# Kernel tuning notes

Measured on AMD Instinct MI355X. Metric: run time of the kernel, lower is better.

Reference implementation:

```python
import jax, jax.numpy as jnp
import numpy as np

N = 16384
D_IN = 64
D_HID = D_IN // 2  # 32
D_OUT = 32


def setup_inputs() -> dict:
    key = jax.random.key(0)
    kA, kX, k1, k2, k3 = jax.random.split(key, 5)
    # Dense adjacency-like operator [N, N]; scaled so activations stay sane.
    A = jax.random.normal(kA, (N, N), dtype=jnp.float32) / np.sqrt(N)
    X = jax.random.normal(kX, (N, D_IN), dtype=jnp.float32)
    # torch nn.Linear weights: [out_features, in_features], no bias
    W1 = jax.random.normal(k1, (D_IN, D_IN), dtype=jnp.float32) / np.sqrt(D_IN)
    W2 = jax.random.normal(k2, (D_HID, D_IN), dtype=jnp.float32) / np.sqrt(D_IN)
    W3 = jax.random.normal(k3, (D_OUT, D_HID), dtype=jnp.float32) / np.sqrt(D_HID)
    return {"A": A, "X": X, "W1": W1, "W2": W2, "W3": W3}


def reference(A, X, W1, W2, W3):
    # Layer 1: relu(fc1(A @ X)); fc(x) = x @ W.T
    h = jax.nn.relu((A @ X) @ W1.T)        # [N, D_IN]
    # Layer 2: relu(fc2(A @ h))
    h = jax.nn.relu((A @ h) @ W2.T)        # [N, D_HID]
    # Layer 3: fc3(A @ h), no activation
    return (A @ h) @ W3.T                  # [N, D_OUT]
```

## Files before the change

kernel.cpp:

```cpp
#include <hip/hip_runtime.h>
#include <cstdint>
#include <cstddef>


#define NN 16384
#define SPLITK 8
#define KCHUNK (NN / SPLITK)

typedef __attribute__((ext_vector_type(8))) short s16x8;
typedef __attribute__((ext_vector_type(4))) float fx4;

__device__ __forceinline__ unsigned short f2bf_rne(float f) {
    unsigned int x = __builtin_bit_cast(unsigned int, f);
    x += 0x7fffu + ((x >> 16) & 1u);
    return (unsigned short)(x >> 16);
}

__device__ __forceinline__ s16x8 pack_bf(fx4 a, fx4 b) {
    s16x8 t;
    t[0] = (short)f2bf_rne(a[0]);
    t[1] = (short)f2bf_rne(a[1]);
    t[2] = (short)f2bf_rne(a[2]);
    t[3] = (short)f2bf_rne(a[3]);
    t[4] = (short)f2bf_rne(b[0]);
    t[5] = (short)f2bf_rne(b[1]);
    t[6] = (short)f2bf_rne(b[2]);
    t[7] = (short)f2bf_rne(b[3]);
    return t;
}

template <int D, int AMODE>
__global__ __launch_bounds__(256, 4) void k_spmm(
    const float* __restrict__ A32,
    const unsigned short* __restrict__ Abf_r,
    unsigned short* __restrict__ Abf_w,
    const unsigned short* __restrict__ PT,
    float* __restrict__ part)
{
    const int lane = threadIdx.x & 63;
    const int wv   = threadIdx.x >> 6;
    const int srow = lane & 15;
    const int kg   = lane >> 4;
    const int s    = blockIdx.y;
    const long kbeg = (long)s * KCHUNK;
    const int rowbase = blockIdx.x * 128 + wv * 32;
    const long r0 = rowbase + srow;
    const long r1 = rowbase + 16 + srow;

    fx4 acc0[D / 16], acc1[D / 16];
#pragma unroll
    for (int c = 0; c < D / 16; ++c) {
        acc0[c] = (fx4){0.f, 0.f, 0.f, 0.f};
        acc1[c] = (fx4){0.f, 0.f, 0.f, 0.f};
    }

#pragma unroll 2
    for (int i = 0; i < KCHUNK / 32; ++i) {
        const long ko = kbeg + (long)i * 32;
        s16x8 af0, af1;
        if (AMODE == 2) {
            af0 = __builtin_nontemporal_load((const s16x8*)(Abf_r + r0 * (long)NN + ko + kg * 8));
            af1 = __builtin_nontemporal_load((const s16x8*)(Abf_r + r1 * (long)NN + ko + kg * 8));
        } else {
            const float* p0 = A32 + r0 * (long)NN + ko + kg * 4;
            const float* p1 = A32 + r1 * (long)NN + ko + kg * 4;
            fx4 a00 = __builtin_nontemporal_load((const fx4*)p0);
            fx4 a01 = __builtin_nontemporal_load((const fx4*)(p0 + 16));
            fx4 a10 = __builtin_nontemporal_load((const fx4*)p1);
            fx4 a11 = __builtin_nontemporal_load((const fx4*)(p1 + 16));
            af0 = pack_bf(a00, a01);
            af1 = pack_bf(a10, a11);
            if (AMODE == 1) {
                __builtin_nontemporal_store(af0, (s16x8*)(Abf_w + r0 * (long)NN + ko + kg * 8));
                __builtin_nontemporal_store(af1, (s16x8*)(Abf_w + r1 * (long)NN + ko + kg * 8));
            }
        }
#pragma unroll
        for (int c = 0; c < D / 16; ++c) {
            s16x8 bf = *(const s16x8*)(PT + (long)(c * 16 + srow) * NN + ko + kg * 8);
            acc0[c] = __builtin_amdgcn_mfma_f32_16x16x32_bf16(af0, bf, acc0[c], 0, 0, 0);
            acc1[c] = __builtin_amdgcn_mfma_f32_16x16x32_bf16(af1, bf, acc1[c], 0, 0, 0);
        }
    }

    float* pbase = part + (long)s * NN * D;
#pragma unroll
    for (int c = 0; c < D / 16; ++c) {
#pragma unroll
        for (int r = 0; r < 4; ++r) {
            pbase[(long)(rowbase + kg * 4 + r) * D + c * 16 + srow]      = acc0[c][r];
            pbase[(long)(rowbase + 16 + kg * 4 + r) * D + c * 16 + srow] = acc1[c][r];
        }
    }
}

template <int DIN, int DOUT, int NSUM, bool RELU>
__global__ __launch_bounds__(256) void k_proj(
    const float* __restrict__ src,
    const float* __restrict__ W,
    unsigned short* __restrict__ PT)
{
    __shared__ float Ws[DOUT * DIN];
    __shared__ float Hs[64][DIN + 1];
    const int tid = threadIdx.x;
    for (int i = tid; i < DOUT * DIN; i += 256) Ws[i] = W[i];
    const int rbase = blockIdx.x * 64;
    for (int i = tid; i < 64 * DIN; i += 256) {
        const int rl = i / DIN, k = i % DIN;
        float v = 0.f;
#pragma unroll
        for (int s2 = 0; s2 < NSUM; ++s2)
            v += src[(long)s2 * NN * DIN + (long)(rbase + rl) * DIN + k];
        Hs[rl][k] = RELU ? fmaxf(v, 0.f) : v;
    }
    __syncthreads();
    const int rl = tid & 63;
    const int c0 = tid >> 6;
    const int r  = rbase + rl;
    const int kk = r & 31;
    const int pidx = (r & ~31) + ((kk & 15) >> 2) * 8 + (kk & 3) + ((kk >> 4) << 2);
    for (int c = c0; c < DOUT; c += 4) {
        float accv = 0.f;
#pragma unroll
        for (int k = 0; k < DIN; ++k) accv += Hs[rl][k] * Ws[c * DIN + k];
        PT[(long)c * NN + pidx] = f2bf_rne(accv);
    }
}

__global__ __launch_bounds__(256) void k_red(
    const float* __restrict__ part, float* __restrict__ out)
{
    const int e = blockIdx.x * 256 + threadIdx.x;
    if (e >= NN * 32 / 4) return;
    fx4 v = (fx4){0.f, 0.f, 0.f, 0.f};
#pragma unroll
    for (int s = 0; s < SPLITK; ++s)
        v += __builtin_nontemporal_load((const fx4*)(part + (long)s * NN * 32 + (long)e * 4));
    *(fx4*)(out + (long)e * 4) = v;
}

extern "C" void kernel_launch(void* const* d_in, const int* in_sizes, int n_in,
                              void* d_out, int out_size, void* d_ws, size_t ws_size,
                              hipStream_t stream) {
    const float* A  = (const float*)d_in[0];
    const float* X  = (const float*)d_in[1];
    const float* W1 = (const float*)d_in[2];
    const float* W2 = (const float*)d_in[3];
    const float* W3 = (const float*)d_in[4];
    float* out = (float*)d_out;

    char* ws = (char*)d_ws;
    const size_t part_b = (size_t)SPLITK * NN * 64 * 4;
    const size_t pt_b   = (size_t)64 * NN * 2;
    const size_t abf_b  = (size_t)NN * NN * 2;
    float*          part = (float*)ws;
    unsigned short* PT   = (unsigned short*)(ws + part_b);
    unsigned short* Abf  = (unsigned short*)(ws + part_b + pt_b);
    const bool save = ws_size >= part_b + pt_b + abf_b;

    dim3 b(256);
    dim3 gP(NN / 64);
    dim3 gG(NN / 128, SPLITK);

    k_proj<64, 64, 1, false><<<gP, b, 0, stream>>>(X, W1, PT);
    if (save) k_spmm<64, 1><<<gG, b, 0, stream>>>(A, nullptr, Abf, PT, part);
    else      k_spmm<64, 0><<<gG, b, 0, stream>>>(A, nullptr, nullptr, PT, part);

    k_proj<64, 32, SPLITK, true><<<gP, b, 0, stream>>>(part, W2, PT);
    if (save) k_spmm<32, 2><<<gG, b, 0, stream>>>(nullptr, Abf, nullptr, PT, part);
    else      k_spmm<32, 0><<<gG, b, 0, stream>>>(A, nullptr, nullptr, PT, part);

    k_proj<32, 32, SPLITK, true><<<gP, b, 0, stream>>>(part, W3, PT);
    if (save) k_spmm<32, 2><<<gG, b, 0, stream>>>(nullptr, Abf, nullptr, PT, part);
    else      k_spmm<32, 0><<<gG, b, 0, stream>>>(A, nullptr, nullptr, PT, part);

    k_red<<<dim3(NN * 32 / 4 / 256), b, 0, stream>>>(part, out);
}
```

Measured before the change: 821.5 us.

## Fuse all GCN stages into one persistent cooperative kernel with grid syncs

Replaces the seven separate launches (three projections, three split-K SpMMs, one reduction) with a single persistent cooperative kernel. Phases are separated by grid-wide barriers and work units are distributed with grid-stride loops. Layers 2 and 3 now use split-K of 16 with 64-row wave tiles, so each PT fragment is reused across four A tiles. This removes launch gaps and tail effects, at the cost of grid-sync overhead, a persistent grid capped by occupancy, and a larger partial-sum reduction.

```diff
diff --git a/kernel.cpp b/kernel.cpp
--- a/kernel.cpp
+++ b/kernel.cpp
@@ -1,11 +1,16 @@
 #include <hip/hip_runtime.h>
+#include <hip/hip_cooperative_groups.h>
 #include <cstdint>
 #include <cstddef>
 
+namespace cg = cooperative_groups;
+
 
 #define NN 16384
-#define SPLITK 8
-#define KCHUNK (NN / SPLITK)
+#define SK1 8
+#define KC1 (NN / SK1)
+#define SK2 16
+#define KC2 (NN / SK2)
 
 typedef __attribute__((ext_vector_type(8))) short s16x8;
 typedef __attribute__((ext_vector_type(4))) float fx4;
@@ -29,114 +34,185 @@
     return t;
 }
 
-template <int D, int AMODE>
-__global__ __launch_bounds__(256, 4) void k_spmm(
-    const float* __restrict__ A32,
-    const unsigned short* __restrict__ Abf_r,
-    unsigned short* __restrict__ Abf_w,
-    const unsigned short* __restrict__ PT,
-    float* __restrict__ part)
-{
-    const int lane = threadIdx.x & 63;
-    const int wv   = threadIdx.x >> 6;
-    const int srow = lane & 15;
-    const int kg   = lane >> 4;
-    const int s    = blockIdx.y;
-    const long kbeg = (long)s * KCHUNK;
-    const int rowbase = blockIdx.x * 128 + wv * 32;
-    const long r0 = rowbase + srow;
-    const long r1 = rowbase + 16 + srow;
-
-    fx4 acc0[D / 16], acc1[D / 16];
-#pragma unroll
-    for (int c = 0; c < D / 16; ++c) {
-        acc0[c] = (fx4){0.f, 0.f, 0.f, 0.f};
-        acc1[c] = (fx4){0.f, 0.f, 0.f, 0.f};
-    }
-
+template <int DIN, int DOUT, int NSUM, bool RELU>
+__device__ __forceinline__ void proj_phase(
+    const float* __restrict__ src, const float* __restrict__ W,
+    unsigned short* __restrict__ PT, float* Ws, float* Hs,
+    int nblk, int bid, int tid)
+{
+    for (int i = tid; i < DOUT * DIN; i += 256) Ws[i] = W[i];
+    for (int rb = bid; rb < NN / 16; rb += nblk) {
+        const int rbase = rb * 16;
+        __syncthreads();
+        for (int i = tid; i < 16 * DIN; i += 256) {
+            const int rl = i / DIN, k = i % DIN;
+            float v = 0.f;
+#pragma unroll
+            for (int s2 = 0; s2 < NSUM; ++s2)
+                v += src[(long)s2 * NN * DIN + (long)(rbase + rl) * DIN + k];
+            Hs[rl * 65 + k] = RELU ? fmaxf(v, 0.f) : v;
+        }
+        __syncthreads();
+        const int rl = tid & 15;
+        const int r = rbase + rl;
+        const int kk = r & 31;
+        const int pidx = (r & ~31) + ((kk & 15) >> 2) * 8 + (kk & 3) + ((kk >> 4) << 2);
+        for (int c = tid >> 4; c < DOUT; c += 16) {
+            float acc = 0.f;
+#pragma unroll
+            for (int k = 0; k < DIN; ++k) acc += Hs[rl * 65 + k] * Ws[c * DIN + k];
+            PT[(long)c * NN + pidx] = f2bf_rne(acc);
+        }
+    }
+}
+
+template <int SAVE>
+__device__ __forceinline__ void spmm1_phase(
+    const float* __restrict__ A32, unsigned short* __restrict__ Abf,
+    const unsigned short* __restrict__ PT, float* __restrict__ part,
+    int nblk, int bid, int wv, int srow, int kg)
+{
+    for (int wu = bid; wu < (NN / 128) * SK1; wu += nblk) {
+        const int rb = wu & (NN / 128 - 1);
+        const int s  = wu >> 7;
+        const long kbeg = (long)s * KC1;
+        const int rowbase = rb * 128 + wv * 32;
+        const long r0 = rowbase + srow;
+        const long r1 = rowbase + 16 + srow;
+
+        fx4 acc0[4], acc1[4];
+#pragma unroll
+        for (int c = 0; c < 4; ++c) {
+            acc0[c] = (fx4){0.f, 0.f, 0.f, 0.f};
+            acc1[c] = (fx4){0.f, 0.f, 0.f, 0.f};
+        }
 #pragma unroll 2
-    for (int i = 0; i < KCHUNK / 32; ++i) {
-        const long ko = kbeg + (long)i * 32;
-        s16x8 af0, af1;
-        if (AMODE == 2) {
-            af0 = __builtin_nontemporal_load((const s16x8*)(Abf_r + r0 * (long)NN + ko + kg * 8));
-            af1 = __builtin_nontemporal_load((const s16x8*)(Abf_r + r1 * (long)NN + ko + kg * 8));
-        } else {
+        for (int i = 0; i < KC1 / 32; ++i) {
+            const long ko = kbeg + (long)i * 32;
             const float* p0 = A32 + r0 * (long)NN + ko + kg * 4;
             const float* p1 = A32 + r1 * (long)NN + ko + kg * 4;
             fx4 a00 = __builtin_nontemporal_load((const fx4*)p0);
             fx4 a01 = __builtin_nontemporal_load((const fx4*)(p0 + 16));
             fx4 a10 = __builtin_nontemporal_load((const fx4*)p1);
             fx4 a11 = __builtin_nontemporal_load((const fx4*)(p1 + 16));
-            af0 = pack_bf(a00, a01);
-            af1 = pack_bf(a10, a11);
-            if (AMODE == 1) {
-                __builtin_nontemporal_store(af0, (s16x8*)(Abf_w + r0 * (long)NN + ko + kg * 8));
-                __builtin_nontemporal_store(af1, (s16x8*)(Abf_w + r1 * (long)NN + ko + kg * 8));
-            }
-        }
-#pragma unroll
-        for (int c = 0; c < D / 16; ++c) {
-            s16x8 bf = *(const s16x8*)(PT + (long)(c * 16 + srow) * NN + ko + kg * 8);
-            acc0[c] = __builtin_amdgcn_mfma_f32_16x16x32_bf16(af0, bf, acc0[c], 0, 0, 0);
-            acc1[c] = __builtin_amdgcn_mfma_f32_16x16x32_bf16(af1, bf, acc1[c], 0, 0, 0);
-        }
-    }
-
-    float* pbase = part + (long)s * NN * D;
-#pragma unroll
-    for (int c = 0; c < D / 16; ++c) {
-#pragma unroll
-        for (int r = 0; r < 4; ++r) {
-            pbase[(long)(rowbase + kg * 4 + r) * D + c * 16 + srow]      = acc0[c][r];
-            pbase[(long)(rowbase + 16 + kg * 4 + r) * D + c * 16 + srow] = acc1[c][r];
-        }
-    }
-}
-
-template <int DIN, int DOUT, int NSUM, bool RELU>
-__global__ __launch_bounds__(256) void k_proj(
-    const float* __restrict__ src,
-    const float* __restrict__ W,
-    unsigned short* __restrict__ PT)
-{
-    __shared__ float Ws[DOUT * DIN];
-    __shared__ float Hs[64][DIN + 1];
-    const int tid = threadIdx.x;
-    for (int i = tid; i < DOUT * DIN; i += 256) Ws[i] = W[i];
-    const int rbase = blockIdx.x * 64;
-    for (int i = tid; i < 64 * DIN; i += 256) {
-        const int rl = i / DIN, k = i % DIN;
-        float v = 0.f;
-#pragma unroll
-        for (int s2 = 0; s2 < NSUM; ++s2)
-            v += src[(long)s2 * NN * DIN + (long)(rbase + rl) * DIN + k];
-        Hs[rl][k] = RELU ? fmaxf(v, 0.f) : v;
-    }
-    __syncthreads();
-    const int rl = tid & 63;
-    const int c0 = tid >> 6;
-    const int r  = rbase + rl;
-    const int kk = r & 31;
-    const int pidx = (r & ~31) + ((kk & 15) >> 2) * 8 + (kk & 3) + ((kk >> 4) << 2);
-    for (int c = c0; c < DOUT; c += 4) {
-        float accv = 0.f;
-#pragma unroll
-        for (int k = 0; k < DIN; ++k) accv += Hs[rl][k] * Ws[c * DIN + k];
-        PT[(long)c * NN + pidx] = f2bf_rne(accv);
-    }
-}
-
-__global__ __launch_bounds__(256) void k_red(
-    const float* __restrict__ part, float* __restrict__ out)
-{
-    const int e = blockIdx.x * 256 + threadIdx.x;
-    if (e >= NN * 32 / 4) return;
-    fx4 v = (fx4){0.f, 0.f, 0.f, 0.f};
-#pragma unroll
-    for (int s = 0; s < SPLITK; ++s)
-        v += __builtin_nontemporal_load((const fx4*)(part + (long)s * NN * 32 + (long)e * 4));
-    *(fx4*)(out + (long)e * 4) = v;
+            s16x8 af0 = pack_bf(a00, a01);
+            s16x8 af1 = pack_bf(a10, a11);
+            if (SAVE) {
+                __builtin_nontemporal_store(af0, (s16x8*)(Abf + r0 * (long)NN + ko + kg * 8));
+                __builtin_nontemporal_store(af1, (s16x8*)(Abf + r1 * (long)NN + ko + kg * 8));
+            }
+#pragma unroll
+            for (int c = 0; c < 4; ++c) {
+                s16x8 bf = *(const s16x8*)(PT + (long)(c * 16 + srow) * NN + ko + kg * 8);
+                acc0[c] = __builtin_amdgcn_mfma_f32_16x16x32_bf16(af0, bf, acc0[c], 0, 0, 0);
+                acc1[c] = __builtin_amdgcn_mfma_f32_16x16x32_bf16(af1, bf, acc1[c], 0, 0, 0);
+            }
+        }
+        float* pbase = part + (long)s * NN * 64;
+#pragma unroll
+        for (int c = 0; c < 4; ++c)
+#pragma unroll
+            for (int r = 0; r < 4; ++r) {
+                pbase[(long)(rowbase + kg * 4 + r) * 64 + c * 16 + srow]      = acc0[c][r];
+                pbase[(long)(rowbase + 16 + kg * 4 + r) * 64 + c * 16 + srow] = acc1[c][r];
+            }
+    }
+}
+
+template <int ABF>
+__device__ __forceinline__ void spmm2_phase(
+    const unsigned short* __restrict__ Abf, const float* __restrict__ A32,
+    const unsigned short* __restrict__ PT, float* __restrict__ part,
+    int nblk, int bid, int wv, int srow, int kg)
+{
+    for (int wu = bid; wu < (NN / 256) * SK2; wu += nblk) {
+        const int rb = wu & (NN / 256 - 1);
+        const int s  = wu >> 6;
+        const long kbeg = (long)s * KC2;
+        const int rowbase = rb * 256 + wv * 64;
+
+        fx4 acc[4][2];
+#pragma unroll
+        for (int t = 0; t < 4; ++t)
+#pragma unroll
+            for (int c = 0; c < 2; ++c) acc[t][c] = (fx4){0.f, 0.f, 0.f, 0.f};
+
+#pragma unroll 2
+        for (int i = 0; i < KC2 / 32; ++i) {
+            const long ko = kbeg + (long)i * 32;
+            s16x8 af[4];
+            if (ABF) {
+#pragma unroll
+                for (int t = 0; t < 4; ++t)
+                    af[t] = *(const s16x8*)(Abf + (long)(rowbase + t * 16 + srow) * NN + ko + kg * 8);
+            } else {
+#pragma unroll
+                for (int t = 0; t < 4; ++t) {
+                    const float* p = A32 + (long)(rowbase + t * 16 + srow) * NN + ko + kg * 4;
+                    fx4 a0 = __builtin_nontemporal_load((const fx4*)p);
+                    fx4 a1 = __builtin_nontemporal_load((const fx4*)(p + 16));
+                    af[t] = pack_bf(a0, a1);
+                }
+            }
+            s16x8 b0 = *(const s16x8*)(PT + (long)srow * NN + ko + kg * 8);
+            s16x8 b1 = *(const s16x8*)(PT + (long)(16 + srow) * NN + ko + kg * 8);
+#pragma unroll
+            for (int t = 0; t < 4; ++t) {
+                acc[t][0] = __builtin_amdgcn_mfma_f32_16x16x32_bf16(af[t], b0, acc[t][0], 0, 0, 0);
+                acc[t][1] = __builtin_amdgcn_mfma_f32_16x16x32_bf16(af[t], b1, acc[t][1], 0, 0, 0);
+            }
+        }
+        float* pbase = part + (long)s * NN * 32;
+#pragma unroll
+        for (int t = 0; t < 4; ++t)
+#pragma unroll
+            for (int c = 0; c < 2; ++c)
+#pragma unroll
+                for (int r = 0; r < 4; ++r)
+                    pbase[(long)(rowbase + t * 16 + kg * 4 + r) * 32 + c * 16 + srow] = acc[t][c][r];
+    }
+}
+
+__device__ __forceinline__ void red_phase(
+    const float* __restrict__ part, float* __restrict__ out, int nthr, int gtid)
+{
+    for (int e = gtid; e < NN * 32 / 4; e += nthr) {
+        fx4 v = (fx4){0.f, 0.f, 0.f, 0.f};
+#pragma unroll
+        for (int s = 0; s < SK2; ++s)
+            v += *(const fx4*)(part + (long)s * NN * 32 + (long)e * 4);
+        *(fx4*)(out + (long)e * 4) = v;
+    }
+}
+
+template <int SAVE>
+__global__ __launch_bounds__(256, 4) void gcn_fused(
+    const float* __restrict__ A32, const float* __restrict__ X,
+    const float* __restrict__ W1, const float* __restrict__ W2,
+    const float* __restrict__ W3, float* __restrict__ out,
+    float* __restrict__ part, unsigned short* __restrict__ PT,
+    unsigned short* __restrict__ Abf)
+{
+    __shared__ float Ws[64 * 64];
+    __shared__ float Hs[16 * 65];
+    cg::grid_group g = cg::this_grid();
+    const int tid = threadIdx.x, bid = blockIdx.x, nblk = gridDim.x;
+    const int lane = tid & 63, wv = tid >> 6;
+    const int srow = lane & 15, kg = lane >> 4;
+
+    proj_phase<64, 64, 1, false>(X, W1, PT, Ws, Hs, nblk, bid, tid);
+    __threadfence(); g.sync();
+    spmm1_phase<SAVE>(A32, Abf, PT, part, nblk, bid, wv, srow, kg);
+    __threadfence(); g.sync();
+    proj_phase<64, 32, SK1, true>(part, W2, PT, Ws, Hs, nblk, bid, tid);
+    __threadfence(); g.sync();
+    spmm2_phase<SAVE>(Abf, A32, PT, part, nblk, bid, wv, srow, kg);
+    __threadfence(); g.sync();
+    proj_phase<32, 32, SK2, true>(part, W3, PT, Ws, Hs, nblk, bid, tid);
+    __threadfence(); g.sync();
+    spmm2_phase<SAVE>(Abf, A32, PT, part, nblk, bid, wv, srow, kg);
+    __threadfence(); g.sync();
+    red_phase(part, out, nblk * 256, bid * 256 + tid);
 }
 
 extern "C" void kernel_launch(void* const* d_in, const int* in_sizes, int n_in,
@@ -150,7 +226,7 @@
     float* out = (float*)d_out;
 
     char* ws = (char*)d_ws;
-    const size_t part_b = (size_t)SPLITK * NN * 64 * 4;
+    const size_t part_b = (size_t)SK2 * NN * 32 * 4;
     const size_t pt_b   = (size_t)64 * NN * 2;
     const size_t abf_b  = (size_t)NN * NN * 2;
     float*          part = (float*)ws;
@@ -158,21 +234,17 @@
     unsigned short* Abf  = (unsigned short*)(ws + part_b + pt_b);
     const bool save = ws_size >= part_b + pt_b + abf_b;
 
-    dim3 b(256);
-    dim3 gP(NN / 64);
-    dim3 gG(NN / 128, SPLITK);
-
-    k_proj<64, 64, 1, false><<<gP, b, 0, stream>>>(X, W1, PT);
-    if (save) k_spmm<64, 1><<<gG, b, 0, stream>>>(A, nullptr, Abf, PT, part);
-    else      k_spmm<64, 0><<<gG, b, 0, stream>>>(A, nullptr, nullptr, PT, part);
-
-    k_proj<64, 32, SPLITK, true><<<gP, b, 0, stream>>>(part, W2, PT);
-    if (save) k_spmm<32, 2><<<gG, b, 0, stream>>>(nullptr, Abf, nullptr, PT, part);
-    else      k_spmm<32, 0><<<gG, b, 0, stream>>>(A, nullptr, nullptr, PT, part);
-
-    k_proj<32, 32, SPLITK, true><<<gP, b, 0, stream>>>(part, W3, PT);
-    if (save) k_spmm<32, 2><<<gG, b, 0, stream>>>(nullptr, Abf, nullptr, PT, part);
-    else      k_spmm<32, 0><<<gG, b, 0, stream>>>(A, nullptr, nullptr, PT, part);
-
-    k_red<<<dim3(NN * 32 / 4 / 256), b, 0, stream>>>(part, out);
-}
+    int maxb = 0;
+    if (save) hipOccupancyMaxActiveBlocksPerMultiprocessor(&maxb, gcn_fused<1>, 256, 0);
+    else      hipOccupancyMaxActiveBlocksPerMultiprocessor(&maxb, gcn_fused<0>, 256, 0);
+    if (maxb < 1) maxb = 1;
+    long cap = (long)maxb * 256;
+    int grid = (int)(cap < 1024 ? cap : 1024);
+
+    void* args[] = {(void*)&A, (void*)&X, (void*)&W1, (void*)&W2, (void*)&W3,
+                    (void*)&out, (void*)&part, (void*)&PT, (void*)&Abf};
+    if (save)
+        hipLaunchCooperativeKernel(gcn_fused<1>, dim3(grid), dim3(256), args, 0, stream);
+    else
+        hipLaunchCooperativeKernel(gcn_fused<0>, dim3(grid), dim3(256), args, 0, stream);
+}
```

After: 1.510 ms. 83.8% more time.

## Store bf16 A in MFMA-fragment tiled layout and retile later SpMM passes

Applied to the files above, without the earlier changes.

The first pass now writes the bf16 copy of A in a fragment-contiguous tiled layout, so each wave's 64 lanes read one contiguous 1 KB block per k-step instead of strided row segments. Layers 2 and 3 use a new kernel in which each wave covers 64 rows (4 A fragments) and reuses two B fragments across them. That kernel uses split-K 16 instead of 8 to keep the grid populated. The partial buffer for 16 splits of width 32 fits within the existing allocation, but the reduce and projection kernels now read twice as many partials.

```diff
diff --git a/kernel.cpp b/kernel.cpp
--- a/kernel.cpp
+++ b/kernel.cpp
@@ -4,8 +4,11 @@
 
 
 #define NN 16384
-#define SPLITK 8
-#define KCHUNK (NN / SPLITK)
+#define SK1 8
+#define KC1 (NN / SK1)
+#define SK2 16
+#define KC2 (NN / SK2)
+#define NKB (NN / 32)
 
 typedef __attribute__((ext_vector_type(8))) short s16x8;
 typedef __attribute__((ext_vector_type(4))) float fx4;
@@ -29,11 +32,10 @@
     return t;
 }
 
-template <int D, int AMODE>
-__global__ __launch_bounds__(256, 4) void k_spmm(
+template <int SAVE>
+__global__ __launch_bounds__(256, 4) void k_spmm1(
     const float* __restrict__ A32,
-    const unsigned short* __restrict__ Abf_r,
-    unsigned short* __restrict__ Abf_w,
+    unsigned short* __restrict__ Abf,
     const unsigned short* __restrict__ PT,
     float* __restrict__ part)
 {
@@ -42,56 +44,108 @@
     const int srow = lane & 15;
     const int kg   = lane >> 4;
     const int s    = blockIdx.y;
-    const long kbeg = (long)s * KCHUNK;
+    const long kbeg = (long)s * KC1;
     const int rowbase = blockIdx.x * 128 + wv * 32;
     const long r0 = rowbase + srow;
     const long r1 = rowbase + 16 + srow;
-
-    fx4 acc0[D / 16], acc1[D / 16];
-#pragma unroll
-    for (int c = 0; c < D / 16; ++c) {
+    const long g0 = rowbase >> 4, g1 = g0 + 1;
+
+    fx4 acc0[4], acc1[4];
+#pragma unroll
+    for (int c = 0; c < 4; ++c) {
         acc0[c] = (fx4){0.f, 0.f, 0.f, 0.f};
         acc1[c] = (fx4){0.f, 0.f, 0.f, 0.f};
     }
 
 #pragma unroll 2
-    for (int i = 0; i < KCHUNK / 32; ++i) {
+    for (int i = 0; i < KC1 / 32; ++i) {
         const long ko = kbeg + (long)i * 32;
-        s16x8 af0, af1;
-        if (AMODE == 2) {
-            af0 = __builtin_nontemporal_load((const s16x8*)(Abf_r + r0 * (long)NN + ko + kg * 8));
-            af1 = __builtin_nontemporal_load((const s16x8*)(Abf_r + r1 * (long)NN + ko + kg * 8));
-        } else {
-            const float* p0 = A32 + r0 * (long)NN + ko + kg * 4;
-            const float* p1 = A32 + r1 * (long)NN + ko + kg * 4;
-            fx4 a00 = __builtin_nontemporal_load((const fx4*)p0);
-            fx4 a01 = __builtin_nontemporal_load((const fx4*)(p0 + 16));
-            fx4 a10 = __builtin_nontemporal_load((const fx4*)p1);
-            fx4 a11 = __builtin_nontemporal_load((const fx4*)(p1 + 16));
-            af0 = pack_bf(a00, a01);
-            af1 = pack_bf(a10, a11);
-            if (AMODE == 1) {
-                __builtin_nontemporal_store(af0, (s16x8*)(Abf_w + r0 * (long)NN + ko + kg * 8));
-                __builtin_nontemporal_store(af1, (s16x8*)(Abf_w + r1 * (long)NN + ko + kg * 8));
-            }
-        }
-#pragma unroll
-        for (int c = 0; c < D / 16; ++c) {
+        const long kblk = ko >> 5;
+        const float* p0 = A32 + r0 * (long)NN + ko + kg * 4;
+        const float* p1 = A32 + r1 * (long)NN + ko + kg * 4;
+        fx4 a00 = __builtin_nontemporal_load((const fx4*)p0);
+        fx4 a01 = __builtin_nontemporal_load((const fx4*)(p0 + 16));
+        fx4 a10 = __builtin_nontemporal_load((const fx4*)p1);
+        fx4 a11 = __builtin_nontemporal_load((const fx4*)(p1 + 16));
+        s16x8 af0 = pack_bf(a00, a01);
+        s16x8 af1 = pack_bf(a10, a11);
+        if (SAVE) {
+            *(s16x8*)(Abf + ((g0 * NKB + kblk) * 64 + lane) * 8) = af0;
+            *(s16x8*)(Abf + ((g1 * NKB + kblk) * 64 + lane) * 8) = af1;
+        }
+#pragma unroll
+        for (int c = 0; c < 4; ++c) {
             s16x8 bf = *(const s16x8*)(PT + (long)(c * 16 + srow) * NN + ko + kg * 8);
             acc0[c] = __builtin_amdgcn_mfma_f32_16x16x32_bf16(af0, bf, acc0[c], 0, 0, 0);
             acc1[c] = __builtin_amdgcn_mfma_f32_16x16x32_bf16(af1, bf, acc1[c], 0, 0, 0);
         }
     }
-
-    float* pbase = part + (long)s * NN * D;
-#pragma unroll
-    for (int c = 0; c < D / 16; ++c) {
+    float* pbase = part + (long)s * NN * 64;
+#pragma unroll
+    for (int c = 0; c < 4; ++c)
 #pragma unroll
         for (int r = 0; r < 4; ++r) {
-            pbase[(long)(rowbase + kg * 4 + r) * D + c * 16 + srow]      = acc0[c][r];
-            pbase[(long)(rowbase + 16 + kg * 4 + r) * D + c * 16 + srow] = acc1[c][r];
-        }
-    }
+            pbase[(long)(rowbase + kg * 4 + r) * 64 + c * 16 + srow]      = acc0[c][r];
+            pbase[(long)(rowbase + 16 + kg * 4 + r) * 64 + c * 16 + srow] = acc1[c][r];
+        }
+}
+
+template <int ABF>
+__global__ __launch_bounds__(256, 4) void k_spmm2(
+    const unsigned short* __restrict__ Abf,
+    const float* __restrict__ A32,
+    const unsigned short* __restrict__ PT,
+    float* __restrict__ part)
+{
+    const int lane = threadIdx.x & 63;
+    const int wv   = threadIdx.x >> 6;
+    const int srow = lane & 15;
+    const int kg   = lane >> 4;
+    const int s    = blockIdx.y;
+    const long kbeg = (long)s * KC2;
+    const int rowbase = blockIdx.x * 256 + wv * 64;
+    const long g0 = rowbase >> 4;
+
+    fx4 acc[4][2];
+#pragma unroll
+    for (int t = 0; t < 4; ++t)
+#pragma unroll
+        for (int c = 0; c < 2; ++c) acc[t][c] = (fx4){0.f, 0.f, 0.f, 0.f};
+
+#pragma unroll 2
+    for (int i = 0; i < KC2 / 32; ++i) {
+        const long ko = kbeg + (long)i * 32;
+        const long kblk = ko >> 5;
+        s16x8 af[4];
+        if (ABF) {
+#pragma unroll
+            for (int t = 0; t < 4; ++t)
+                af[t] = *(const s16x8*)(Abf + (((g0 + t) * NKB + kblk) * 64 + lane) * 8);
+        } else {
+#pragma unroll
+            for (int t = 0; t < 4; ++t) {
+                const float* p = A32 + (long)(rowbase + t * 16 + srow) * NN + ko + kg * 4;
+                fx4 a0 = __builtin_nontemporal_load((const fx4*)p);
+                fx4 a1 = __builtin_nontemporal_load((const fx4*)(p + 16));
+                af[t] = pack_bf(a0, a1);
+            }
+        }
+        s16x8 b0 = *(const s16x8*)(PT + (long)srow * NN + ko + kg * 8);
+        s16x8 b1 = *(const s16x8*)(PT + (long)(16 + srow) * NN + ko + kg * 8);
+#pragma unroll
+        for (int t = 0; t < 4; ++t) {
+            acc[t][0] = __builtin_amdgcn_mfma_f32_16x16x32_bf16(af[t], b0, acc[t][0], 0, 0, 0);
+            acc[t][1] = __builtin_amdgcn_mfma_f32_16x16x32_bf16(af[t], b1, acc[t][1], 0, 0, 0);
+        }
+    }
+    float* pbase = part + (long)s * NN * 32;
+#pragma unroll
+    for (int t = 0; t < 4; ++t)
+#pragma unroll
+        for (int c = 0; c < 2; ++c)
+#pragma unroll
+            for (int r = 0; r < 4; ++r)
+                pbase[(long)(rowbase + t * 16 + kg * 4 + r) * 32 + c * 16 + srow] = acc[t][c][r];
 }
 
 template <int DIN, int DOUT, int NSUM, bool RELU>
@@ -134,8 +188,8 @@
     if (e >= NN * 32 / 4) return;
     fx4 v = (fx4){0.f, 0.f, 0.f, 0.f};
 #pragma unroll
-    for (int s = 0; s < SPLITK; ++s)
-        v += __builtin_nontemporal_load((const fx4*)(part + (long)s * NN * 32 + (long)e * 4));
+    for (int s = 0; s < SK2; ++s)
+        v += *(const fx4*)(part + (long)s * NN * 32 + (long)e * 4);
     *(fx4*)(out + (long)e * 4) = v;
 }
 
@@ -150,7 +204,7 @@
     float* out = (float*)d_out;
 
     char* ws = (char*)d_ws;
-    const size_t part_b = (size_t)SPLITK * NN * 64 * 4;
+    const size_t part_b = (size_t)SK1 * NN * 64 * 4;
     const size_t pt_b   = (size_t)64 * NN * 2;
     const size_t abf_b  = (size_t)NN * NN * 2;
     float*          part = (float*)ws;
@@ -160,19 +214,20 @@
 
     dim3 b(256);
     dim3 gP(NN / 64);
-    dim3 gG(NN / 128, SPLITK);
+    dim3 g1(NN / 128, SK1);
+    dim3 g2(NN / 256, SK2);
 
     k_proj<64, 64, 1, false><<<gP, b, 0, stream>>>(X, W1, PT);
-    if (save) k_spmm<64, 1><<<gG, b, 0, stream>>>(A, nullptr, Abf, PT, part);
-    else      k_spmm<64, 0><<<gG, b, 0, stream>>>(A, nullptr, nullptr, PT, part);
-
-    k_proj<64, 32, SPLITK, true><<<gP, b, 0, stream>>>(part, W2, PT);
-    if (save) k_spmm<32, 2><<<gG, b, 0, stream>>>(nullptr, Abf, nullptr, PT, part);
-    else      k_spmm<32, 0><<<gG, b, 0, stream>>>(A, nullptr, nullptr, PT, part);
-
-    k_proj<32, 32, SPLITK, true><<<gP, b, 0, stream>>>(part, W3, PT);
-    if (save) k_spmm<32, 2><<<gG, b, 0, stream>>>(nullptr, Abf, nullptr, PT, part);
-    else      k_spmm<32, 0><<<gG, b, 0, stream>>>(A, nullptr, nullptr, PT, part);
+    if (save) k_spmm1<1><<<g1, b, 0, stream>>>(A, Abf, PT, part);
+    else      k_spmm1<0><<<g1, b, 0, stream>>>(A, Abf, PT, part);
+
+    k_proj<64, 32, SK1, true><<<gP, b, 0, stream>>>(part, W2, PT);
+    if (save) k_spmm2<1><<<g2, b, 0, stream>>>(Abf, A, PT, part);
+    else      k_spmm2<0><<<g2, b, 0, stream>>>(Abf, A, PT, part);
+
+    k_proj<32, 32, SK2, true><<<gP, b, 0, stream>>>(part, W3, PT);
+    if (save) k_spmm2<1><<<g2, b, 0, stream>>>(Abf, A, PT, part);
+    else      k_spmm2<0><<<g2, b, 0, stream>>>(Abf, A, PT, part);
 
     k_red<<<dim3(NN * 32 / 4 / 256), b, 0, stream>>>(part, out);
 }
```

Result: faster. 689.5 us (-16.1%).
